# Kernel optimization log

Hardware: AMD Instinct MI355X
Metric: run time of the kernel (lower is better)

The kernel has to match this reference:

```python
import jax, jax.numpy as jnp
import numpy as np
import math

B, S, H = 2, 2048, 2048
NH, HD = 16, 128           # num_heads, head_dim; num_kv_heads == num_heads (MHA)
THETA = 10000.0


def setup_inputs() -> dict:
    key = jax.random.key(0)
    ks = jax.random.split(key, 5)
    scale = 0.02
    hidden_states = jax.random.normal(ks[0], (B, S, H), jnp.float32)
    q_w = jax.random.normal(ks[1], (H, H), jnp.float32) * scale
    k_w = jax.random.normal(ks[2], (H, H), jnp.float32) * scale
    v_w = jax.random.normal(ks[3], (H, H), jnp.float32) * scale
    o_w = jax.random.normal(ks[4], (H, H), jnp.float32) * scale
    # additive causal mask, finite large-negative (as HF builds it)
    causal = jnp.tril(jnp.ones((S, S), bool))
    attention_mask = jnp.where(causal, 0.0, -1e9).astype(jnp.float32)[None, None]  # [1,1,S,S]
    position_ids = jnp.broadcast_to(jnp.arange(S, dtype=jnp.int64), (B, S))
    return {
        "hidden_states": hidden_states,
        "q_w": q_w, "k_w": k_w, "v_w": v_w, "o_w": o_w,
        "attention_mask": attention_mask,
        "position_ids": position_ids,
    }


def _rotate_half(x):
    x1, x2 = x[..., : x.shape[-1] // 2], x[..., x.shape[-1] // 2 :]
    return jnp.concatenate((-x2, x1), axis=-1)


def _rope_cos_sin(position_ids):
    inv_freq = 1.0 / (THETA ** (jnp.arange(0, HD, 2, dtype=jnp.float32) / HD))  # [HD/2]
    freqs = position_ids.astype(jnp.float32)[:, :, None] * inv_freq[None, None, :]  # [B,S,HD/2]
    emb = jnp.concatenate((freqs, freqs), axis=-1)  # [B,S,HD]
    # unsqueeze head dim (unsqueeze_dim=1 after transpose to [B,H,S,D])
    return jnp.cos(emb)[:, None], jnp.sin(emb)[:, None]  # [B,1,S,HD]


def reference(hidden_states, q_w, k_w, v_w, o_w, attention_mask, position_ids):
    # projections (torch Linear: y = x @ W^T), split heads -> [B,NH,S,HD]
    def proj(w):
        return jnp.einsum('bsh,oh->bso', hidden_states, w).reshape(B, S, NH, HD).transpose(0, 2, 1, 3)
    q, k, v = proj(q_w), proj(k_w), proj(v_w)

    cos, sin = _rope_cos_sin(position_ids)
    q = q * cos + _rotate_half(q) * sin
    k = k * cos + _rotate_half(k) * sin

    scores = jnp.einsum('bhqd,bhkd->bhqk', q, k) / math.sqrt(HD)  # [B,NH,S,S]
    scores = scores + attention_mask
    attn = jax.nn.softmax(scores, axis=-1)  # dropout p=0.0 -> identity
    out = jnp.einsum('bhqk,bhkd->bhqd', attn, v)  # [B,NH,S,HD]
    out = out.transpose(0, 2, 1, 3).reshape(B, S, H)
    return jnp.einsum('bsh,oh->bso', out, o_w)
```

## Files before the change

### kernel.cpp

```cpp
#include <hip/hip_runtime.h>
#include <hip/hip_bf16.h>

using bf16 = __hip_bfloat16;
typedef short  short8  __attribute__((ext_vector_type(8)));
typedef float  float4_ __attribute__((ext_vector_type(4)));
typedef int    int4_   __attribute__((ext_vector_type(4)));

typedef __attribute__((address_space(1))) const void* gas_ptr;
typedef __attribute__((address_space(3))) void*       las_ptr;

#define MFMA_BF16(a, b, c) __builtin_amdgcn_mfma_f32_16x16x32_bf16((a), (b), (c), 0, 0, 0)

__device__ __forceinline__ float bf2f(bf16 v) { return __bfloat162float(v); }
__device__ __forceinline__ bf16  f2bf(float v) { return __float2bfloat16(v); }

__global__ __launch_bounds__(256)
void cvt_all(const float* __restrict__ X,  const float* __restrict__ Wq,
             const float* __restrict__ Wk, const float* __restrict__ Wv,
             const float* __restrict__ Wo,
             bf16* __restrict__ Xb,  bf16* __restrict__ Wqb,
             bf16* __restrict__ Wkb, bf16* __restrict__ Wvb,
             bf16* __restrict__ Wob)
{
    const size_t i = ((size_t)blockIdx.x * 256 + threadIdx.x) * 8;
    const float* src; bf16* dst; size_t off;
    if (i < 8388608)       { src = X;  dst = Xb;  off = i; }
    else if (i < 12582912) { src = Wq; dst = Wqb; off = i - 8388608; }
    else if (i < 16777216) { src = Wk; dst = Wkb; off = i - 12582912; }
    else if (i < 20971520) { src = Wv; dst = Wvb; off = i - 16777216; }
    else                   { src = Wo; dst = Wob; off = i - 20971520; }
    const float4_ a = *(const float4_*)(src + off);
    const float4_ b = *(const float4_*)(src + off + 4);
    union { short8 s; bf16 h[8]; } u;
#pragma unroll
    for (int j = 0; j < 4; ++j) { u.h[j] = f2bf(a[j]); u.h[j + 4] = f2bf(b[j]); }
    *(short8*)(dst + off) = u.s;
}

__global__ __launch_bounds__(256)
void gemm128(const bf16* __restrict__ A,
             const bf16* __restrict__ W0, const bf16* __restrict__ W1, const bf16* __restrict__ W2,
             bf16* __restrict__ O0, bf16* __restrict__ O1, bf16* __restrict__ O2,
             float* __restrict__ OF, int mode)
{
    constexpr int K = 2048;
    const int z = blockIdx.z;
    const bf16* W  = (z == 0) ? W0 : (z == 1) ? W1 : W2;
    bf16*      Out = (z == 0) ? O0 : (z == 1) ? O1 : O2;

    const int bm = blockIdx.y * 128;
    const int bn = blockIdx.x * 128;

    const int tid  = threadIdx.x;
    const int wave = tid >> 6;
    const int ln   = tid & 63;
    const int r15  = ln & 15;
    const int quad = ln >> 4;
    const int wr   = wave >> 1, wc = wave & 1;

    __shared__ bf16 As[128 * 32];
    __shared__ bf16 Bs[128 * 32];

    float4_ acc[4][4];
    const float4_ fzero = {0.f, 0.f, 0.f, 0.f};
#pragma unroll
    for (int i = 0; i < 4; ++i)
#pragma unroll
        for (int j = 0; j < 4; ++j) acc[i][j] = fzero;

    const int srow = ln >> 2;
    const int scg  = (ln & 3) * 8;

    for (int kt = 0; kt < K / 32; ++kt) {
        const int k0 = kt * 32;
#pragma unroll
        for (int c = 0; c < 2; ++c) {
            const int rb = (wave * 2 + c) * 16;
            const bf16* ga = A + (size_t)(bm + rb + srow) * K + k0 + scg;
            const bf16* gb = W + (size_t)(bn + rb + srow) * K + k0 + scg;
            __builtin_amdgcn_global_load_lds((gas_ptr)ga, (las_ptr)(&As[rb * 32]), 16, 0, 0);
            __builtin_amdgcn_global_load_lds((gas_ptr)gb, (las_ptr)(&Bs[rb * 32]), 16, 0, 0);
        }
        __syncthreads();

        short8 af[4], bfr[4];
#pragma unroll
        for (int i = 0; i < 4; ++i)
            af[i] = *(const short8*)&As[(wr * 64 + i * 16 + r15) * 32 + quad * 8];
#pragma unroll
        for (int j = 0; j < 4; ++j)
            bfr[j] = *(const short8*)&Bs[(wc * 64 + j * 16 + r15) * 32 + quad * 8];
#pragma unroll
        for (int i = 0; i < 4; ++i)
#pragma unroll
            for (int j = 0; j < 4; ++j)
                acc[i][j] = MFMA_BF16(af[i], bfr[j], acc[i][j]);
        __syncthreads();
    }

#pragma unroll
    for (int i = 0; i < 4; ++i) {
#pragma unroll
        for (int j = 0; j < 4; ++j) {
#pragma unroll
            for (int r = 0; r < 4; ++r) {
                const int row = bm + wr * 64 + i * 16 + quad * 4 + r;
                const int col = bn + wc * 64 + j * 16 + r15;
                const float v = acc[i][j][r];
                if (mode == 0) {
                    const int b = row >> 11, s = row & 2047;
                    const int h = col >> 7,  d = col & 127;
                    Out[(((size_t)b * 16 + h) * 2048 + s) * 128 + d] = f2bf(v);
                } else {
                    OF[(size_t)row * 2048 + col] = v;
                }
            }
        }
    }
}

__global__ __launch_bounds__(256)
void rope_scale(bf16* __restrict__ Q, bf16* __restrict__ Kb)
{
    const int idx = blockIdx.x * 256 + threadIdx.x;
    const int d  = idx & 63;
    const int s  = (idx >> 6) & 2047;
    const int bh = idx >> 17;
    const size_t base = ((size_t)bh * 2048 + s) * 128;

    const float inv_freq = expf(-(float)d * (9.210340371976184f / 64.f));
    const float ang = (float)s * inv_freq;
    const float c = cosf(ang), sn = sinf(ang);
    const float sc = 0.08838834764831845f;

    const float q1 = bf2f(Q[base + d]), q2 = bf2f(Q[base + d + 64]);
    Q[base + d]      = f2bf((q1 * c - q2 * sn) * sc);
    Q[base + d + 64] = f2bf((q2 * c + q1 * sn) * sc);

    const float k1 = bf2f(Kb[base + d]), k2 = bf2f(Kb[base + d + 64]);
    Kb[base + d]      = f2bf(k1 * c - k2 * sn);
    Kb[base + d + 64] = f2bf(k2 * c + k1 * sn);
}

__global__ __launch_bounds__(512)
void flash_attn(const bf16* __restrict__ Qg, const bf16* __restrict__ Kg,
                const bf16* __restrict__ Vg, bf16* __restrict__ Og)
{
    constexpr int S = 2048;
    const int qb = blockIdx.x;
    const int bh = blockIdx.y;
    const int b = bh >> 4, h = bh & 15;
    const size_t base = (size_t)bh * S * 128;
    const bf16* Qp = Qg + base;
    const bf16* Kp = Kg + base;
    const bf16* Vp = Vg + base;

    const int tid  = threadIdx.x;
    const int wave = tid >> 6;
    const int ln   = tid & 63;
    const int r15  = ln & 15;
    const int quad = ln >> 4;

    __shared__ bf16 Ks[64][136];
    __shared__ bf16 Vt[128][72];
    __shared__ bf16 Ps[8][16][72];

    const int qs    = qb * 128;
    const int qrow0 = qs + wave * 16;
    const int dt    = qrow0 >> 6;
    const int ktmax = 2 * qb + 1;

    short8 qf[4];
#pragma unroll
    for (int ks = 0; ks < 4; ++ks)
        qf[ks] = *(const short8*)&Qp[(size_t)(qrow0 + r15) * 128 + ks * 32 + quad * 8];

    float4_ acc_o[8];
    const float4_ fzero = {0.f, 0.f, 0.f, 0.f};
#pragma unroll
    for (int of = 0; of < 8; ++of) acc_o[of] = fzero;
    float m_run[4], l_run[4];
#pragma unroll
    for (int r = 0; r < 4; ++r) { m_run[r] = -__builtin_inff(); l_run[r] = 0.f; }

    const int kr = tid >> 4;
    const int kc = (tid & 15) * 8;
    const int vd = wave * 16;

    {
#pragma unroll
        for (int p = 0; p < 2; ++p)
            *(int4_*)&Ks[kr + p * 32][kc] =
                *(const int4_*)&Kp[(size_t)(kr + p * 32) * 128 + kc];
        union { int4_ v; bf16 h[8]; } u;
#pragma unroll
        for (int p = 0; p < 2; ++p) {
            u.v = *(const int4_*)&Vp[(size_t)ln * 128 + vd + p * 8];
#pragma unroll
            for (int j = 0; j < 8; ++j)
                Vt[vd + p * 8 + j][ln] = u.h[j];
        }
    }
    __syncthreads();

    for (int kt = 0; kt <= ktmax; ++kt) {
        const bool more = (kt < ktmax);

        int4_ kpre0, kpre1, vpre0, vpre1;
        if (more) {
            const int krow = (kt + 1) * 64;
            kpre0 = *(const int4_*)&Kp[(size_t)(krow + kr) * 128 + kc];
            kpre1 = *(const int4_*)&Kp[(size_t)(krow + kr + 32) * 128 + kc];
            vpre0 = *(const int4_*)&Vp[(size_t)(krow + ln) * 128 + vd];
            vpre1 = *(const int4_*)&Vp[(size_t)(krow + ln) * 128 + vd + 8];
        }

        if (kt <= dt) {
            float4_ sacc[4];
            __builtin_amdgcn_s_setprio(1);
#pragma unroll
            for (int nf = 0; nf < 4; ++nf) {
                sacc[nf] = fzero;
#pragma unroll
                for (int ks = 0; ks < 4; ++ks) {
                    short8 kf = *(const short8*)&Ks[nf * 16 + r15][ks * 32 + quad * 8];
                    sacc[nf] = MFMA_BF16(qf[ks], kf, sacc[nf]);
                }
            }
            __builtin_amdgcn_s_setprio(0);

            if (kt == dt) {
                const int ro = (qrow0 & 63) + quad * 4;
#pragma unroll
                for (int nf = 0; nf < 4; ++nf) {
                    const int col = nf * 16 + r15;
#pragma unroll
                    for (int r = 0; r < 4; ++r)
                        if (col > ro + r) sacc[nf][r] = -__builtin_inff();
                }
            }

            float mnew[4], alpha[4];
#pragma unroll
            for (int r = 0; r < 4; ++r) {
                float rm = fmaxf(fmaxf(sacc[0][r], sacc[1][r]),
                                 fmaxf(sacc[2][r], sacc[3][r]));
                rm = fmaxf(rm, __shfl_xor(rm, 1));
                rm = fmaxf(rm, __shfl_xor(rm, 2));
                rm = fmaxf(rm, __shfl_xor(rm, 4));
                rm = fmaxf(rm, __shfl_xor(rm, 8));
                mnew[r]  = fmaxf(m_run[r], rm);
                alpha[r] = __expf(m_run[r] - mnew[r]);
                m_run[r] = mnew[r];
            }
            float rs[4] = {0.f, 0.f, 0.f, 0.f};
#pragma unroll
            for (int nf = 0; nf < 4; ++nf) {
#pragma unroll
                for (int r = 0; r < 4; ++r) {
                    const float p = __expf(sacc[nf][r] - mnew[r]);
                    rs[r] += p;
                    Ps[wave][quad * 4 + r][nf * 16 + r15] = f2bf(p);
                }
            }
#pragma unroll
            for (int r = 0; r < 4; ++r) {
                float t = rs[r];
                t += __shfl_xor(t, 1);
                t += __shfl_xor(t, 2);
                t += __shfl_xor(t, 4);
                t += __shfl_xor(t, 8);
                l_run[r] = l_run[r] * alpha[r] + t;
            }
#pragma unroll
            for (int of = 0; of < 8; ++of)
#pragma unroll
                for (int r = 0; r < 4; ++r)
                    acc_o[of][r] *= alpha[r];

            __builtin_amdgcn_s_setprio(1);
#pragma unroll
            for (int k2 = 0; k2 < 2; ++k2) {
                short8 pf = *(const short8*)&Ps[wave][r15][k2 * 32 + quad * 8];
#pragma unroll
                for (int of = 0; of < 8; ++of) {
                    short8 vf = *(const short8*)&Vt[of * 16 + r15][k2 * 32 + quad * 8];
                    acc_o[of] = MFMA_BF16(pf, vf, acc_o[of]);
                }
            }
            __builtin_amdgcn_s_setprio(0);
        }

        __syncthreads();
        if (more) {
            *(int4_*)&Ks[kr][kc]      = kpre0;
            *(int4_*)&Ks[kr + 32][kc] = kpre1;
            union { int4_ v; bf16 h[8]; } u;
            u.v = vpre0;
#pragma unroll
            for (int j = 0; j < 8; ++j) Vt[vd + j][ln] = u.h[j];
            u.v = vpre1;
#pragma unroll
            for (int j = 0; j < 8; ++j) Vt[vd + 8 + j][ln] = u.h[j];
        }
        __syncthreads();
    }

#pragma unroll
    for (int r = 0; r < 4; ++r) {
        const float inv = 1.f / l_run[r];
        const int  s  = qrow0 + quad * 4 + r;
        const size_t ob = (((size_t)b * S + s) * 16 + h) * 128;
#pragma unroll
        for (int of = 0; of < 8; ++of)
            Og[ob + of * 16 + r15] = f2bf(acc_o[of][r] * inv);
    }
}

extern "C" void kernel_launch(void* const* d_in, const int* in_sizes, int n_in,
                              void* d_out, int out_size, void* d_ws, size_t ws_size,
                              hipStream_t stream)
{
    const float* X  = (const float*)d_in[0];
    const float* Wq = (const float*)d_in[1];
    const float* Wk = (const float*)d_in[2];
    const float* Wv = (const float*)d_in[3];
    const float* Wo = (const float*)d_in[4];
    float* out = (float*)d_out;

    bf16* Xb  = (bf16*)d_ws;
    bf16* Wqb = Xb  + 8388608;
    bf16* Wkb = Wqb + 4194304;
    bf16* Wvb = Wkb + 4194304;
    bf16* Wob = Wvb + 4194304;
    bf16* q   = Wob + 4194304;
    bf16* k   = q   + 8388608;
    bf16* v   = k   + 8388608;
    bf16* ao  = v   + 8388608;

    dim3 blk(256);
    cvt_all<<<dim3(12288), blk, 0, stream>>>(X, Wq, Wk, Wv, Wo,
                                             Xb, Wqb, Wkb, Wvb, Wob);
    gemm128<<<dim3(16, 32, 3), blk, 0, stream>>>(Xb, Wqb, Wkb, Wvb,
                                                 q, k, v, nullptr, 0);
    rope_scale<<<dim3((2 * 16 * 2048 * 64) / 256), blk, 0, stream>>>(q, k);
    flash_attn<<<dim3(16, 32), dim3(512), 0, stream>>>(q, k, v, ao);
    gemm128<<<dim3(16, 32, 1), blk, 0, stream>>>(ao, Wob, Wob, Wob,
                                                 nullptr, nullptr, nullptr, out, 1);
}
```

Before: 514.1 us.

## Replace 128x128 GEMM with 256x256 double-buffered pipelined GEMM kernel

Result: slower. 541.5 us (+5.3%).

```diff
diff --git a/kernel.cpp b/kernel.cpp
--- a/kernel.cpp
+++ b/kernel.cpp
@@ -13,6 +13,9 @@
 
 __device__ __forceinline__ float bf2f(bf16 v) { return __bfloat162float(v); }
 __device__ __forceinline__ bf16  f2bf(float v) { return __float2bfloat16(v); }
+
+#define BAR() do { asm volatile("" ::: "memory"); __builtin_amdgcn_s_barrier(); asm volatile("" ::: "memory"); } while (0)
+#define WAITLGKM0() asm volatile("s_waitcnt lgkmcnt(0)" ::: "memory")
 
 __global__ __launch_bounds__(256)
 void cvt_all(const float* __restrict__ X,  const float* __restrict__ Wq,
@@ -37,86 +40,147 @@
     *(short8*)(dst + off) = u.s;
 }
 
-__global__ __launch_bounds__(256)
-void gemm128(const bf16* __restrict__ A,
-             const bf16* __restrict__ W0, const bf16* __restrict__ W1, const bf16* __restrict__ W2,
-             bf16* __restrict__ O0, bf16* __restrict__ O1, bf16* __restrict__ O2,
-             float* __restrict__ OF, int mode)
+__global__ __launch_bounds__(512, 2)
+void gemm256(const bf16* __restrict__ Ap, const bf16* __restrict__ Wp,
+             bf16* __restrict__ Oq, float* __restrict__ OF, int mode)
 {
-    constexpr int K = 2048;
-    const int z = blockIdx.z;
-    const bf16* W  = (z == 0) ? W0 : (z == 1) ? W1 : W2;
-    bf16*      Out = (z == 0) ? O0 : (z == 1) ? O1 : O2;
-
-    const int bm = blockIdx.y * 128;
-    const int bn = blockIdx.x * 128;
+    constexpr int NT = 32;
+    __shared__ bf16 As0[2 * 256 * 64];
+    __shared__ bf16 Bs0[2 * 256 * 64];
+
+    const int nwg  = gridDim.x * gridDim.y;
+    const int bid0 = blockIdx.y * gridDim.x + blockIdx.x;
+    const int cpx  = nwg >> 3;
+    const int swzb = (bid0 & 7) * cpx + (bid0 >> 3);
+    const int bn = (swzb % gridDim.x) * 256;
+    const int bm = (swzb / gridDim.x) * 256;
 
     const int tid  = threadIdx.x;
-    const int wave = tid >> 6;
+    const int w    = tid >> 6;
     const int ln   = tid & 63;
     const int r15  = ln & 15;
     const int quad = ln >> 4;
-    const int wr   = wave >> 1, wc = wave & 1;
-
-    __shared__ bf16 As[128 * 32];
-    __shared__ bf16 Bs[128 * 32];
-
-    float4_ acc[4][4];
+    const int wr   = w >> 2;
+    const int wc   = w & 3;
+
+    const int srow = ln >> 3;
+    const int scol = ((ln & 7) ^ (ln >> 3)) * 8;
+    const int w8   = w * 8;
+    const int cx   = (r15 & 7) * 8;
+
+#define STAGE_A(pb, ts, qm) do {                                            \
+    _Pragma("unroll")                                                       \
+    for (int c = 0; c < 2; ++c) {                                           \
+        const int rl = c * 128 + (qm) * 64 + w8;                            \
+        __builtin_amdgcn_global_load_lds(                                   \
+            (gas_ptr)(Ap + (size_t)(bm + rl + srow) * 2048 + (ts) * 64 + scol), \
+            (las_ptr)(As0 + (pb) * 16384 + rl * 64), 16, 0, 0);             \
+    } } while (0)
+
+#define STAGE_B(pb, ts, qn) do {                                            \
+    _Pragma("unroll")                                                       \
+    for (int c = 0; c < 2; ++c) {                                           \
+        const int rl = (c * 2 + (w >> 2)) * 64 + (qn) * 32 + (w & 3) * 8;   \
+        __builtin_amdgcn_global_load_lds(                                   \
+            (gas_ptr)(Wp + (size_t)(bn + rl + srow) * 2048 + (ts) * 64 + scol), \
+            (las_ptr)(Bs0 + (pb) * 16384 + rl * 64), 16, 0, 0);             \
+    } } while (0)
+
+#define LDA(qm) do {                                                        \
+    _Pragma("unroll")                                                       \
+    for (int i = 0; i < 4; ++i) {                                           \
+        const int row = wr * 128 + (qm) * 64 + i * 16 + r15;                \
+        a[i][0] = *(const short8*)(As0 + p * 16384 + row * 64 + ((quad * 8) ^ cx));      \
+        a[i][1] = *(const short8*)(As0 + p * 16384 + row * 64 + ((32 + quad * 8) ^ cx)); \
+    } } while (0)
+
+#define LDB(qn) do {                                                        \
+    _Pragma("unroll")                                                       \
+    for (int j = 0; j < 2; ++j) {                                           \
+        const int row = wc * 64 + (qn) * 32 + j * 16 + r15;                 \
+        b[j][0] = *(const short8*)(Bs0 + p * 16384 + row * 64 + ((quad * 8) ^ cx));      \
+        b[j][1] = *(const short8*)(Bs0 + p * 16384 + row * 64 + ((32 + quad * 8) ^ cx)); \
+    } } while (0)
+
+#define MM(qm, qn) do {                                                     \
+    __builtin_amdgcn_s_setprio(1);                                          \
+    _Pragma("unroll")                                                       \
+    for (int i = 0; i < 4; ++i)                                             \
+        _Pragma("unroll")                                                   \
+        for (int j = 0; j < 2; ++j)                                         \
+            _Pragma("unroll")                                               \
+            for (int kk = 0; kk < 2; ++kk)                                  \
+                acc[(qm) * 4 + i][(qn) * 2 + j] =                           \
+                    MFMA_BF16(a[i][kk], b[j][kk], acc[(qm) * 4 + i][(qn) * 2 + j]); \
+    __builtin_amdgcn_s_setprio(0); } while (0)
+
+    float4_ acc[8][4];
     const float4_ fzero = {0.f, 0.f, 0.f, 0.f};
 #pragma unroll
-    for (int i = 0; i < 4; ++i)
+    for (int i = 0; i < 8; ++i)
 #pragma unroll
         for (int j = 0; j < 4; ++j) acc[i][j] = fzero;
 
-    const int srow = ln >> 2;
-    const int scg  = (ln & 3) * 8;
-
-    for (int kt = 0; kt < K / 32; ++kt) {
-        const int k0 = kt * 32;
-#pragma unroll
-        for (int c = 0; c < 2; ++c) {
-            const int rb = (wave * 2 + c) * 16;
-            const bf16* ga = A + (size_t)(bm + rb + srow) * K + k0 + scg;
-            const bf16* gb = W + (size_t)(bn + rb + srow) * K + k0 + scg;
-            __builtin_amdgcn_global_load_lds((gas_ptr)ga, (las_ptr)(&As[rb * 32]), 16, 0, 0);
-            __builtin_amdgcn_global_load_lds((gas_ptr)gb, (las_ptr)(&Bs[rb * 32]), 16, 0, 0);
-        }
-        __syncthreads();
-
-        short8 af[4], bfr[4];
-#pragma unroll
-        for (int i = 0; i < 4; ++i)
-            af[i] = *(const short8*)&As[(wr * 64 + i * 16 + r15) * 32 + quad * 8];
-#pragma unroll
-        for (int j = 0; j < 4; ++j)
-            bfr[j] = *(const short8*)&Bs[(wc * 64 + j * 16 + r15) * 32 + quad * 8];
-#pragma unroll
-        for (int i = 0; i < 4; ++i)
-#pragma unroll
-            for (int j = 0; j < 4; ++j)
-                acc[i][j] = MFMA_BF16(af[i], bfr[j], acc[i][j]);
-        __syncthreads();
+    short8 a[4][2], b[2][2];
+
+    STAGE_A(0, 0, 0); STAGE_B(0, 0, 0); STAGE_B(0, 0, 1); STAGE_A(0, 0, 1);
+    STAGE_A(1, 1, 0); STAGE_B(1, 1, 1); STAGE_A(1, 1, 1);
+    asm volatile("s_waitcnt vmcnt(6)" ::: "memory");
+    BAR();
+
+    for (int t = 0; t < NT; ++t) {
+        const int p = t & 1, pq = p ^ 1;
+        LDA(0); LDB(0);
+        if (t + 1 < NT) STAGE_B(pq, t + 1, 0);
+        asm volatile("s_waitcnt lgkmcnt(8)" ::: "memory");
+        BAR(); WAITLGKM0();
+        MM(0, 0);
+        BAR();
+        LDB(1);
+        if (t + 2 < NT) STAGE_A(p, t + 2, 0);
+        BAR(); WAITLGKM0();
+        MM(0, 1);
+        BAR();
+        LDA(1);
+        if (t + 2 < NT) STAGE_B(p, t + 2, 1);
+        BAR(); WAITLGKM0();
+        MM(1, 1);
+        BAR();
+        LDB(0);
+        if (t + 2 < NT) STAGE_A(p, t + 2, 1);
+        BAR(); WAITLGKM0();
+        MM(1, 0);
+        if (t == NT - 2) { asm volatile("s_waitcnt vmcnt(0)" ::: "memory"); }
+        else             { asm volatile("s_waitcnt vmcnt(6)" ::: "memory"); }
+        BAR();
     }
-
-#pragma unroll
-    for (int i = 0; i < 4; ++i) {
-#pragma unroll
-        for (int j = 0; j < 4; ++j) {
+    asm volatile("s_waitcnt vmcnt(0)" ::: "memory");
+
+#pragma unroll
+    for (int mi = 0; mi < 8; ++mi) {
+#pragma unroll
+        for (int ni = 0; ni < 4; ++ni) {
 #pragma unroll
             for (int r = 0; r < 4; ++r) {
-                const int row = bm + wr * 64 + i * 16 + quad * 4 + r;
-                const int col = bn + wc * 64 + j * 16 + r15;
-                const float v = acc[i][j][r];
+                const int row = bm + wr * 128 + mi * 16 + quad * 4 + r;
+                const int col = bn + wc * 64 + ni * 16 + r15;
+                const float v = acc[mi][ni][r];
                 if (mode == 0) {
-                    const int b = row >> 11, s = row & 2047;
-                    const int h = col >> 7,  d = col & 127;
-                    Out[(((size_t)b * 16 + h) * 2048 + s) * 128 + d] = f2bf(v);
+                    const int z = col >> 11, c2 = col & 2047;
+                    const int h = c2 >> 7, d = c2 & 127;
+                    const int bb = row >> 11, s = row & 2047;
+                    Oq[(size_t)z * 8388608 + (((size_t)bb * 16 + h) * 2048 + s) * 128 + d] = f2bf(v);
                 } else {
                     OF[(size_t)row * 2048 + col] = v;
                 }
             }
         }
     }
+#undef STAGE_A
+#undef STAGE_B
+#undef LDA
+#undef LDB
+#undef MM
 }
 
 __global__ __launch_bounds__(256)
@@ -341,10 +405,8 @@
     dim3 blk(256);
     cvt_all<<<dim3(12288), blk, 0, stream>>>(X, Wq, Wk, Wv, Wo,
                                              Xb, Wqb, Wkb, Wvb, Wob);
-    gemm128<<<dim3(16, 32, 3), blk, 0, stream>>>(Xb, Wqb, Wkb, Wvb,
-                                                 q, k, v, nullptr, 0);
+    gemm256<<<dim3(24, 16), dim3(512), 0, stream>>>(Xb, Wqb, q, nullptr, 0);
     rope_scale<<<dim3((2 * 16 * 2048 * 64) / 256), blk, 0, stream>>>(q, k);
     flash_attn<<<dim3(16, 32), dim3(512), 0, stream>>>(q, k, v, ao);
-    gemm128<<<dim3(16, 32, 1), blk, 0, stream>>>(ao, Wob, Wob, Wob,
-                                                 nullptr, nullptr, nullptr, out, 1);
+    gemm256<<<dim3(8, 16), dim3(512), 0, stream>>>(ao, Wob, nullptr, out, 1);
 }
```
